# Optimization experiments

Measured on AMD Instinct MI355X. Metric: run time of the kernel, lower is better.

## Reference

```python
import jax, jax.numpy as jnp
import numpy as np

B, S, D, N, K = 2, 2048, 512, 32768, 64
CHUNK = 2048  # min(2048, num_slots) as in the torch source
EPS = 1e-8


def _phase_linear(x, Wr, Wi, br, bi):
    # complex linear on [..., d, 2] phase tensors
    xr, xi = x[..., 0], x[..., 1]
    yr = xr @ Wr.T - xi @ Wi.T + br
    yi = xr @ Wi.T + xi @ Wr.T + bi
    return jnp.stack([yr, yi], axis=-1)


def _phase_norm(x, gamma):
    # RMS normalization of the complex magnitude over dim, scaled by gamma
    mag2 = (x * x).sum(-1)                      # [..., d]
    rms = jnp.sqrt(mag2.mean(-1, keepdims=True) + EPS)
    return x * (gamma / rms)[..., None]


def setup_inputs() -> dict:
    key = jax.random.key(0)
    ks = jax.random.split(key, 8)
    inp = {
        'query': jax.random.normal(ks[0], (B, S, D, 2), jnp.float32),
        'keys': jax.random.normal(ks[1], (N, D, 2), jnp.float32) * 0.02,
        'values': jax.random.normal(ks[2], (N, D, 2), jnp.float32) * 0.02,
        'Wq_r': jax.random.normal(ks[3], (D, D), jnp.float32) * 0.02,
        'Wq_i': jax.random.normal(ks[4], (D, D), jnp.float32) * 0.02,
        'bq_r': jnp.zeros((D,), jnp.float32),
        'bq_i': jnp.zeros((D,), jnp.float32),
        'Wo_r': jax.random.normal(ks[5], (D, D), jnp.float32) * 0.02,
        'Wo_i': jax.random.normal(ks[6], (D, D), jnp.float32) * 0.02,
        'bo_r': jnp.zeros((D,), jnp.float32),
        'bo_i': jnp.zeros((D,), jnp.float32),
        'ln_gamma': jnp.ones((D,), jnp.float32),
        'top_k': K,
    }
    return inp


def _read(query, keys, values, Wq_r, Wq_i, bq_r, bq_i, Wo_r, Wo_i, bo_r, bo_i, ln_gamma, top_k):
    b, s, d, _ = query.shape
    n = keys.shape[0]
    q = _phase_linear(query, Wq_r, Wq_i, bq_r, bq_i)
    qf = q.reshape(b * s, d, 2)
    q_r, q_i = qf[..., 0], qf[..., 1]
    q_mag = jnp.sqrt((q_r * q_r + q_i * q_i).sum(-1) + EPS)  # [Q]
    nq = b * s

    n_chunks = n // CHUNK
    key_chunks = keys.reshape(n_chunks, CHUNK, d, 2)
    offsets = jnp.arange(n_chunks, dtype=jnp.int32) * CHUNK
    local_idx = jnp.arange(CHUNK, dtype=jnp.int32)

    def body(carry, xs):
        tv, ti = carry                      # [Q, K], [Q, K]
        ck, off = xs                        # [C, d, 2], scalar
        k_r, k_i = ck[..., 0], ck[..., 1]
        k_mag = jnp.sqrt((k_r * k_r + k_i * k_i).sum(-1) + EPS)   # [C]
        coh = q_r @ k_r.T + q_i @ k_i.T                            # [Q, C]
        coh = coh / (q_mag[:, None] * k_mag[None, :] + EPS)
        idx = jnp.broadcast_to(off + local_idx, (nq, CHUNK))
        cv = jnp.concatenate([tv, coh], axis=-1)
        ci = jnp.concatenate([ti, idx], axis=-1)
        nv, loc = jax.lax.top_k(cv, top_k)
        ni = jnp.take_along_axis(ci, loc, axis=-1)
        return (nv, ni), None

    init = (jnp.full((nq, top_k), -jnp.inf, jnp.float32),
            jnp.zeros((nq, top_k), jnp.int32))
    (topk_vals, topk_idx), _ = jax.lax.scan(body, init, (key_chunks, offsets))

    attn = jax.nn.softmax(topk_vals, axis=-1)                      # [Q, K]
    gathered = values[topk_idx]                                    # [Q, K, d, 2]
    retrieved = jnp.einsum('qk,qkdp->qdp', attn, gathered).reshape(b, s, d, 2)

    out = _phase_norm(retrieved, ln_gamma)
    out = _phase_linear(out, Wo_r, Wo_i, bo_r, bo_i)
    return out


def reference(query, keys, values, Wq_r, Wq_i, bq_r, bq_i, Wo_r, Wo_i, bo_r, bo_i, ln_gamma, top_k):
    return _read(query, keys, values, Wq_r, Wq_i, bq_r, bq_i, Wo_r, Wo_i, bo_r, bo_i, ln_gamma, top_k)
```

## Files before the change

### kernel.cpp

```cpp
#include <hip/hip_runtime.h>
#include <math.h>
#include <float.h>

#define EPSF 1e-8f
#define EPSD 1e-8
#define D_DIM 512
#define T_DIM 1024
#define K_TOP 64
#define K_KEEP 128
#define NBIN 2048
#define CAND_SORT 1024

typedef __bf16 bf16_t;
typedef __bf16 bf16x8 __attribute__((ext_vector_type(8)));
typedef __bf16 bf16x4 __attribute__((ext_vector_type(4)));
typedef float f32x4 __attribute__((ext_vector_type(4)));

__global__ __launch_bounds__(256)
void rownorm_convert_q_kernel(const double* __restrict__ X, double* __restrict__ magd,
                              bf16_t* __restrict__ Qn, int rows) {
  int r = blockIdx.x;
  if (r >= rows) return;
  int tid = threadIdx.x;
  const double* xr = X + (size_t)r * T_DIM;
  double v[4];
  double s = 0.0;
  #pragma unroll
  for (int i = 0; i < 4; i++) { v[i] = xr[tid * 4 + i]; s += v[i] * v[i]; }
  for (int o = 32; o > 0; o >>= 1) s += __shfl_down(s, o, 64);
  __shared__ double red[4];
  __shared__ double mag_s;
  if ((tid & 63) == 0) red[tid >> 6] = s;
  __syncthreads();
  if (tid == 0) {
    double m = sqrt(red[0] + red[1] + red[2] + red[3] + EPSD);
    magd[r] = m; mag_s = m;
  }
  __syncthreads();
  double inv = 1.0 / mag_s;
  bf16x4 o;
  #pragma unroll
  for (int i = 0; i < 4; i++) o[i] = (bf16_t)((float)(v[i] * inv));
  *(bf16x4*)(Qn + (size_t)r * T_DIM + tid * 4) = o;
}

__global__ __launch_bounds__(256)
void rownorm_convert_k_kernel(const float* __restrict__ X, double* __restrict__ magd,
                              bf16_t* __restrict__ Kn, int rows) {
  int r = blockIdx.x;
  if (r >= rows) return;
  int tid = threadIdx.x;
  float4 v = ((const float4*)(X + (size_t)r * T_DIM))[tid];
  double s = (double)v.x * v.x + (double)v.y * v.y + (double)v.z * v.z + (double)v.w * v.w;
  for (int o = 32; o > 0; o >>= 1) s += __shfl_down(s, o, 64);
  __shared__ double red[4];
  __shared__ float inv_s;
  if ((tid & 63) == 0) red[tid >> 6] = s;
  __syncthreads();
  if (tid == 0) {
    double m = sqrt(red[0] + red[1] + red[2] + red[3] + EPSD);
    magd[r] = m; inv_s = (float)(1.0 / m);
  }
  __syncthreads();
  float inv = inv_s;
  bf16x4 o;
  o[0] = (bf16_t)(v.x * inv); o[1] = (bf16_t)(v.y * inv);
  o[2] = (bf16_t)(v.z * inv); o[3] = (bf16_t)(v.w * inv);
  *(bf16x4*)(Kn + (size_t)r * T_DIM + tid * 4) = o;
}

__global__ __launch_bounds__(256)
void cgemm_f64_kernel(const float* __restrict__ X,
                      const float* __restrict__ Wr, const float* __restrict__ Wi,
                      const float* __restrict__ br, const float* __restrict__ bi,
                      double* __restrict__ Yd, int M) {
  __shared__ float Ar[16][64], Ai[16][64], Br_[16][64], Bi_[16][64];
  int tid = threadIdx.x;
  int tx = tid & 15, ty = tid >> 4;
  int m0 = blockIdx.x * 64, n0 = blockIdx.y * 64;
  double accR[4][4] = {{0}}, accI[4][4] = {{0}};
  for (int k0 = 0; k0 < D_DIM; k0 += 16) {
    #pragma unroll
    for (int gi = 0; gi < 2; gi++) {
      int g = tid + gi * 256;
      int m = g >> 3, dg = g & 7;
      float4 v = *(const float4*)(X + (size_t)(m0 + m) * T_DIM + 2 * k0 + dg * 4);
      Ar[dg*2][m] = v.x; Ai[dg*2][m] = v.y; Ar[dg*2+1][m] = v.z; Ai[dg*2+1][m] = v.w;
    }
    {
      int j = tid >> 2, c = tid & 3;
      float4 vr = *(const float4*)(Wr + (size_t)(n0 + j) * D_DIM + k0 + c * 4);
      float4 vi = *(const float4*)(Wi + (size_t)(n0 + j) * D_DIM + k0 + c * 4);
      Br_[c*4+0][j] = vr.x; Br_[c*4+1][j] = vr.y; Br_[c*4+2][j] = vr.z; Br_[c*4+3][j] = vr.w;
      Bi_[c*4+0][j] = vi.x; Bi_[c*4+1][j] = vi.y; Bi_[c*4+2][j] = vi.z; Bi_[c*4+3][j] = vi.w;
    }
    __syncthreads();
    #pragma unroll
    for (int k = 0; k < 16; k++) {
      float arr[4], aii[4], wrr[4], wii[4];
      *(float4*)arr = *(const float4*)&Ar[k][ty*4];
      *(float4*)aii = *(const float4*)&Ai[k][ty*4];
      *(float4*)wrr = *(const float4*)&Br_[k][tx*4];
      *(float4*)wii = *(const float4*)&Bi_[k][tx*4];
      #pragma unroll
      for (int im = 0; im < 4; im++)
        #pragma unroll
        for (int jn = 0; jn < 4; jn++) {
          double ar = (double)arr[im], ai = (double)aii[im];
          double wr = (double)wrr[jn], wi = (double)wii[jn];
          accR[im][jn] += ar * wr - ai * wi;
          accI[im][jn] += ar * wi + ai * wr;
        }
    }
    __syncthreads();
  }
  #pragma unroll
  for (int im = 0; im < 4; im++) {
    int m = m0 + ty * 4 + im;
    #pragma unroll
    for (int jn = 0; jn < 4; jn++) {
      int j = n0 + tx * 4 + jn;
      size_t base = (size_t)m * T_DIM + j * 2;
      Yd[base]     = accR[im][jn] + (double)br[j];
      Yd[base + 1] = accI[im][jn] + (double)bi[j];
    }
  }
}

__global__ __launch_bounds__(256)
void cgemm_kernel(const float* __restrict__ X,
                  const float* __restrict__ Wr, const float* __restrict__ Wi,
                  const float* __restrict__ br, const float* __restrict__ bi,
                  float* __restrict__ Y, int M) {
  __shared__ float Ar[16][64], Ai[16][64], Br_[16][64], Bi_[16][64];
  int tid = threadIdx.x;
  int tx = tid & 15, ty = tid >> 4;
  int m0 = blockIdx.x * 64, n0 = blockIdx.y * 64;
  float accR[4][4] = {{0}}, accI[4][4] = {{0}};
  for (int k0 = 0; k0 < D_DIM; k0 += 16) {
    #pragma unroll
    for (int gi = 0; gi < 2; gi++) {
      int g = tid + gi * 256;
      int m = g >> 3, dg = g & 7;
      float4 v = *(const float4*)(X + (size_t)(m0 + m) * T_DIM + 2 * k0 + dg * 4);
      Ar[dg*2][m] = v.x; Ai[dg*2][m] = v.y; Ar[dg*2+1][m] = v.z; Ai[dg*2+1][m] = v.w;
    }
    {
      int j = tid >> 2, c = tid & 3;
      float4 vr = *(const float4*)(Wr + (size_t)(n0 + j) * D_DIM + k0 + c * 4);
      float4 vi = *(const float4*)(Wi + (size_t)(n0 + j) * D_DIM + k0 + c * 4);
      Br_[c*4+0][j] = vr.x; Br_[c*4+1][j] = vr.y; Br_[c*4+2][j] = vr.z; Br_[c*4+3][j] = vr.w;
      Bi_[c*4+0][j] = vi.x; Bi_[c*4+1][j] = vi.y; Bi_[c*4+2][j] = vi.z; Bi_[c*4+3][j] = vi.w;
    }
    __syncthreads();
    #pragma unroll
    for (int k = 0; k < 16; k++) {
      float arr[4], aii[4], wrr[4], wii[4];
      *(float4*)arr = *(const float4*)&Ar[k][ty*4];
      *(float4*)aii = *(const float4*)&Ai[k][ty*4];
      *(float4*)wrr = *(const float4*)&Br_[k][tx*4];
      *(float4*)wii = *(const float4*)&Bi_[k][tx*4];
      #pragma unroll
      for (int im = 0; im < 4; im++)
        #pragma unroll
        for (int jn = 0; jn < 4; jn++) {
          accR[im][jn] += arr[im] * wrr[jn] - aii[im] * wii[jn];
          accI[im][jn] += arr[im] * wii[jn] + aii[im] * wrr[jn];
        }
    }
    __syncthreads();
  }
  #pragma unroll
  for (int im = 0; im < 4; im++) {
    int m = m0 + ty * 4 + im;
    #pragma unroll
    for (int jn = 0; jn < 4; jn++) {
      int j = n0 + tx * 4 + jn;
      float2 o; o.x = accR[im][jn] + br[j]; o.y = accI[im][jn] + bi[j];
      *(float2*)(Y + (size_t)m * T_DIM + j * 2) = o;
    }
  }
}

__global__ __launch_bounds__(256)
void mfma_score_kernel(const bf16_t* __restrict__ Qn, const bf16_t* __restrict__ Kn,
                       bf16_t* __restrict__ S, int n_off, int C) {
  __shared__ bf16_t As[128 * 32];
  __shared__ bf16_t Bs[128 * 32];
  int tid = threadIdx.x;
  int lane = tid & 63, wv = tid >> 6;
  int m0 = blockIdx.x * 128;
  int n0 = blockIdx.y * 128;
  int wm = (wv & 1) * 64, wn = (wv >> 1) * 64;
  f32x4 acc[4][4] = {};
  const bf16_t* Ag = Qn + (size_t)m0 * T_DIM;
  const bf16_t* Bg = Kn + (size_t)(n_off + n0) * T_DIM;
  int frow = lane & 15;
  int fk = (lane >> 4) * 8;
  for (int k0 = 0; k0 < T_DIM; k0 += 32) {
    #pragma unroll
    for (int it = 0; it < 2; it++) {
      int rbase = (it * 4 + wv) * 16;
      int row = rbase + (lane >> 2);
      int gcol = lane & 3;
      const bf16_t* gpa = Ag + (size_t)row * T_DIM + k0 + gcol * 8;
      const bf16_t* gpb = Bg + (size_t)row * T_DIM + k0 + gcol * 8;
      bf16_t* lpa = As + rbase * 32 + lane * 8;
      bf16_t* lpb = Bs + rbase * 32 + lane * 8;
      __builtin_amdgcn_global_load_lds(
          (const __attribute__((address_space(1))) void*)gpa,
          (__attribute__((address_space(3))) void*)lpa, 16, 0, 0);
      __builtin_amdgcn_global_load_lds(
          (const __attribute__((address_space(1))) void*)gpb,
          (__attribute__((address_space(3))) void*)lpb, 16, 0, 0);
    }
    __syncthreads();
    bf16x8 a[4], b[4];
    #pragma unroll
    for (int i = 0; i < 4; i++)
      a[i] = *(const bf16x8*)(As + (wm + i * 16 + frow) * 32 + fk);
    #pragma unroll
    for (int j = 0; j < 4; j++)
      b[j] = *(const bf16x8*)(Bs + (wn + j * 16 + frow) * 32 + fk);
    #pragma unroll
    for (int i = 0; i < 4; i++)
      #pragma unroll
      for (int j = 0; j < 4; j++)
        acc[i][j] = __builtin_amdgcn_mfma_f32_16x16x32_bf16(a[i], b[j], acc[i][j], 0, 0, 0);
    __syncthreads();
  }
  int col = lane & 15, qr = (lane >> 4) * 4;
  #pragma unroll
  for (int i = 0; i < 4; i++)
    #pragma unroll
    for (int j = 0; j < 4; j++) {
      int n = n0 + wn + j * 16 + col;
      #pragma unroll
      for (int r = 0; r < 4; r++) {
        int m = m0 + wm + i * 16 + qr + r;
        S[(size_t)m * C + n] = (bf16_t)acc[i][j][r];
      }
    }
}

__global__ __launch_bounds__(256)
void select_kernel(const bf16_t* __restrict__ S, int C, int key_off,
                   float* __restrict__ cand_v, int* __restrict__ cand_i,
                   int slot_off, int nslot) {
  int q = blockIdx.x, tid = threadIdx.x;
  __shared__ unsigned hist[NBIN];
  __shared__ unsigned psum[256];
  __shared__ float bv[CAND_SORT];
  __shared__ int bi[CAND_SORT];
  __shared__ unsigned binB_s, cntGt_s, binB2_s, cnt_s;
  const bf16x8* row8 = (const bf16x8*)(S + (size_t)q * C);
  int nvec = C >> 3;

  for (int i = tid; i < NBIN; i += 256) hist[i] = 0;
  if (tid == 0) { cnt_s = 0; binB_s = 0; cntGt_s = 0; binB2_s = 0; }
  __syncthreads();
  for (int v = tid; v < nvec; v += 256) {
    bf16x8 x = row8[v];
    #pragma unroll
    for (int i = 0; i < 8; i++) {
      unsigned t = __float_as_uint((float)x[i]);
      t = (t & 0x80000000u) ? ~t : (t | 0x80000000u);
      atomicAdd(&hist[t >> 21], 1u);
    }
  }
  __syncthreads();
  unsigned sgrp = 0;
  #pragma unroll
  for (int b = 0; b < 8; b++) sgrp += hist[tid * 8 + b];
  psum[tid] = sgrp;
  __syncthreads();
  for (int off = 1; off < 256; off <<= 1) {
    unsigned v = psum[tid];
    unsigned add = (tid + off < 256) ? psum[tid + off] : 0u;
    __syncthreads();
    psum[tid] = v + add;
    __syncthreads();
  }
  if (psum[tid] >= (unsigned)K_KEEP && (tid == 255 || psum[tid + 1] < (unsigned)K_KEEP)) {
    unsigned acc = (tid == 255) ? 0u : psum[tid + 1];
    for (int b = tid * 8 + 7; b >= tid * 8; b--) {
      unsigned h = hist[b];
      if (acc + h >= (unsigned)K_KEEP) { binB_s = (unsigned)b; cntGt_s = acc; break; }
      acc += h;
    }
  }
  __syncthreads();
  unsigned B = binB_s;
  unsigned K2 = (unsigned)K_KEEP - cntGt_s;
  for (int i = tid; i < NBIN; i += 256) hist[i] = 0;
  __syncthreads();
  for (int v = tid; v < nvec; v += 256) {
    bf16x8 x = row8[v];
    #pragma unroll
    for (int i = 0; i < 8; i++) {
      unsigned t = __float_as_uint((float)x[i]);
      t = (t & 0x80000000u) ? ~t : (t | 0x80000000u);
      if ((t >> 21) == B) atomicAdd(&hist[(t >> 10) & 2047u], 1u);
    }
  }
  __syncthreads();
  unsigned sgrp2 = 0;
  #pragma unroll
  for (int b = 0; b < 8; b++) sgrp2 += hist[tid * 8 + b];
  psum[tid] = sgrp2;
  __syncthreads();
  for (int off = 1; off < 256; off <<= 1) {
    unsigned v = psum[tid];
    unsigned add = (tid + off < 256) ? psum[tid + off] : 0u;
    __syncthreads();
    psum[tid] = v + add;
    __syncthreads();
  }
  if (psum[tid] >= K2 && (tid == 255 || psum[tid + 1] < K2)) {
    unsigned acc = (tid == 255) ? 0u : psum[tid + 1];
    for (int b = tid * 8 + 7; b >= tid * 8; b--) {
      unsigned h = hist[b];
      if (acc + h >= K2) { binB2_s = (unsigned)b; break; }
      acc += h;
    }
  }
  __syncthreads();
  unsigned B2 = binB2_s;
  for (int v = tid; v < nvec; v += 256) {
    bf16x8 x = row8[v];
    #pragma unroll
    for (int i = 0; i < 8; i++) {
      float fx = (float)x[i];
      unsigned t = __float_as_uint(fx);
      t = (t & 0x80000000u) ? ~t : (t | 0x80000000u);
      unsigned bin = t >> 21;
      bool keep = (bin > B) || (bin == B && ((t >> 10) & 2047u) >= B2);
      if (keep) {
        unsigned p = atomicAdd(&cnt_s, 1u);
        if (p < (unsigned)CAND_SORT) { bv[p] = fx; bi[p] = key_off + v * 8 + i; }
      }
    }
  }
  __syncthreads();
  int cnt = (int)min(cnt_s, (unsigned)CAND_SORT);
  int n = K_KEEP; while (n < cnt) n <<= 1;
  for (int x = cnt + tid; x < n; x += 256) { bv[x] = -FLT_MAX; bi[x] = 0x7FFFFFFF; }
  for (int k = 2; k <= n; k <<= 1) {
    for (int j = k >> 1; j > 0; j >>= 1) {
      __syncthreads();
      for (int i = tid; i < n; i += 256) {
        int ixj = i ^ j;
        if (ixj > i) {
          float a = bv[i], b = bv[ixj];
          int ia = bi[i], ib = bi[ixj];
          bool a_worse = (a < b) || (a == b && ia > ib);
          bool up = ((i & k) == 0);
          if (up ? a_worse : !a_worse) {
            bv[i] = b; bv[ixj] = a; bi[i] = ib; bi[ixj] = ia;
          }
        }
      }
    }
  }
  __syncthreads();
  if (tid < K_KEEP) {
    cand_v[(size_t)q * nslot + slot_off + tid] = bv[tid];
    cand_i[(size_t)q * nslot + slot_off + tid] = bi[tid];
  }
}

__global__ __launch_bounds__(256)
void merge_kernel(const float* __restrict__ cand_v, const int* __restrict__ cand_i,
                  int nslot, int* __restrict__ topi) {
  int q = blockIdx.x, tid = threadIdx.x;
  __shared__ float bv[NBIN];
  __shared__ int bi[NBIN];
  int n = K_KEEP; while (n < nslot) n <<= 1;
  for (int i = tid; i < n; i += 256) {
    if (i < nslot) { bv[i] = cand_v[(size_t)q * nslot + i]; bi[i] = cand_i[(size_t)q * nslot + i]; }
    else { bv[i] = -FLT_MAX; bi[i] = 0x7FFFFFFF; }
  }
  for (int k = 2; k <= n; k <<= 1) {
    for (int j = k >> 1; j > 0; j >>= 1) {
      __syncthreads();
      for (int i = tid; i < n; i += 256) {
        int ixj = i ^ j;
        if (ixj > i) {
          float a = bv[i], b = bv[ixj];
          int ia = bi[i], ib = bi[ixj];
          bool a_worse = (a < b) || (a == b && ia > ib);
          bool up = ((i & k) == 0);
          if (up ? a_worse : !a_worse) {
            bv[i] = b; bv[ixj] = a; bi[i] = ib; bi[ixj] = ia;
          }
        }
      }
    }
  }
  __syncthreads();
  if (tid < K_KEEP) topi[q * K_KEEP + tid] = bi[tid];
}

__global__ __launch_bounds__(256)
void rescore_kernel(const int* __restrict__ topi,
                    const double* __restrict__ Qd,
                    const double* __restrict__ qmagd, const double* __restrict__ kmagd,
                    const float* __restrict__ Kk, const float* __restrict__ V,
                    const float* __restrict__ gamma,
                    float* __restrict__ XN) {
  int q = blockIdx.x, tid = threadIdx.x;
  __shared__ double qrow[T_DIM];
  __shared__ double cval[K_KEEP];
  __shared__ int cidx[K_KEEP];
  __shared__ float w[K_TOP];
  __shared__ int widx[K_TOP];
  __shared__ float red[4];
  for (int i = tid; i < T_DIM / 2; i += 256)
    ((double2*)qrow)[i] = ((const double2*)(Qd + (size_t)q * T_DIM))[i];
  if (tid < K_KEEP) cidx[tid] = topi[q * K_KEEP + tid];
  __syncthreads();
  double qm = qmagd[q];
  int wv = tid >> 6, ln = tid & 63;
  #pragma unroll 2
  for (int c = wv; c < K_KEEP; c += 4) {
    int key = cidx[c];
    const float4* kr4 = (const float4*)(Kk + (size_t)key * T_DIM);
    double s = 0.0;
    #pragma unroll
    for (int it = 0; it < 4; it++) {
      float4 v = kr4[ln + it * 64];
      int t = (ln + it * 64) * 4;
      s += (double)v.x * qrow[t]     + (double)v.y * qrow[t + 1]
         + (double)v.z * qrow[t + 2] + (double)v.w * qrow[t + 3];
    }
    for (int o = 32; o > 0; o >>= 1) s += __shfl_down(s, o, 64);
    if (ln == 0) cval[c] = s / (qm * kmagd[key] + EPSD);
  }
  __syncthreads();
  for (int k = 2; k <= K_KEEP; k <<= 1) {
    for (int j = k >> 1; j > 0; j >>= 1) {
      __syncthreads();
      if (tid < K_KEEP) {
        int i = tid, ixj = i ^ j;
        if (ixj > i) {
          double a = cval[i], b = cval[ixj];
          int ia = cidx[i], ib = cidx[ixj];
          bool a_worse = (a < b) || (a == b && ia > ib);
          bool up = ((i & k) == 0);
          if (up ? a_worse : !a_worse) {
            cval[i] = b; cval[ixj] = a; cidx[i] = ib; cidx[ixj] = ia;
          }
        }
      }
    }
  }
  __syncthreads();
  if (tid < 64) {
    double v = cval[tid];
    double m = cval[0];
    double e = exp(v - m);
    double s = e;
    for (int o = 32; o > 0; o >>= 1) s += __shfl_down(s, o, 64);
    s = __shfl(s, 0, 64);
    w[tid] = (float)(e / s);
    widx[tid] = cidx[tid];
  }
  __syncthreads();
  float4 acc = {0.f, 0.f, 0.f, 0.f};
  #pragma unroll 8
  for (int j2 = 0; j2 < 64; j2++) {
    float wj = w[j2];
    float4 v = *(const float4*)(V + (size_t)widx[j2] * T_DIM + tid * 4);
    acc.x += wj * v.x; acc.y += wj * v.y; acc.z += wj * v.z; acc.w += wj * v.w;
  }
  float ls = acc.x*acc.x + acc.y*acc.y + acc.z*acc.z + acc.w*acc.w;
  for (int o = 32; o > 0; o >>= 1) ls += __shfl_down(ls, o, 64);
  if ((tid & 63) == 0) red[tid >> 6] = ls;
  __syncthreads();
  float tot = red[0] + red[1] + red[2] + red[3];
  float rms = sqrtf(tot / (float)D_DIM + EPSF);
  float g0 = gamma[tid * 2] / rms, g1 = gamma[tid * 2 + 1] / rms;
  float4 o = { acc.x * g0, acc.y * g0, acc.z * g1, acc.w * g1 };
  *(float4*)(XN + (size_t)q * T_DIM + tid * 4) = o;
}

extern "C" void kernel_launch(void* const* d_in, const int* in_sizes, int n_in,
                              void* d_out, int out_size, void* d_ws, size_t ws_size,
                              hipStream_t stream) {
  const float* query  = (const float*)d_in[0];
  const float* keys   = (const float*)d_in[1];
  const float* values = (const float*)d_in[2];
  const float* Wq_r   = (const float*)d_in[3];
  const float* Wq_i   = (const float*)d_in[4];
  const float* bq_r   = (const float*)d_in[5];
  const float* bq_i   = (const float*)d_in[6];
  const float* Wo_r   = (const float*)d_in[7];
  const float* Wo_i   = (const float*)d_in[8];
  const float* bo_r   = (const float*)d_in[9];
  const float* bo_i   = (const float*)d_in[10];
  const float* gamma  = (const float*)d_in[11];
  float* out = (float*)d_out;

  int M = in_sizes[0] / T_DIM;
  int N = in_sizes[1] / T_DIM;

  char* ws = (char*)d_ws;
  size_t off = 0;
  double* qd    = (double*)(ws + off); off += (size_t)M * T_DIM * 8;
  float*  xn    = (float*) (ws + off); off += (size_t)M * T_DIM * 4;
  double* qmagd = (double*)(ws + off); off += (size_t)M * 8;
  double* kmagd = (double*)(ws + off); off += (size_t)N * 8;
  int*    topi  = (int*)   (ws + off); off += (size_t)M * K_KEEP * 4;
  bf16_t* qn    = (bf16_t*)(ws + off); off += (size_t)M * T_DIM * 2;
  bf16_t* kn    = (bf16_t*)(ws + off); off += (size_t)N * T_DIM * 2;

  int C = 2048;
  for (int c = N; c >= 2048; c >>= 1) {
    size_t need = off + (size_t)M * c * 2
                + 2 * (size_t)M * (size_t)(N / c) * K_KEEP * 4;
    if (need <= ws_size) { C = c; break; }
  }
  if (C > N) C = N;
  int nchunks = N / C;
  int nslot = nchunks * K_KEEP;

  bf16_t* sc    = (bf16_t*)(ws + off); off += (size_t)M * C * 2;
  float*  candv = (float*) (ws + off); off += (size_t)M * nslot * 4;
  int*    candi = (int*)   (ws + off); off += (size_t)M * nslot * 4;

  dim3 blk(256);
  cgemm_f64_kernel<<<dim3(M / 64, D_DIM / 64), blk, 0, stream>>>(query, Wq_r, Wq_i, bq_r, bq_i, qd, M);
  rownorm_convert_q_kernel<<<dim3(M), blk, 0, stream>>>(qd, qmagd, qn, M);
  rownorm_convert_k_kernel<<<dim3(N), blk, 0, stream>>>(keys, kmagd, kn, N);
  for (int c = 0; c < nchunks; c++) {
    int noff = c * C;
    mfma_score_kernel<<<dim3(M / 128, C / 128), blk, 0, stream>>>(qn, kn, sc, noff, C);
    select_kernel<<<dim3(M), blk, 0, stream>>>(sc, C, noff, candv, candi, c * K_KEEP, nslot);
  }
  merge_kernel<<<dim3(M), blk, 0, stream>>>(candv, candi, nslot, topi);
  rescore_kernel<<<dim3(M), blk, 0, stream>>>(topi, qd, qmagd, kmagd, keys, values, gamma, xn);
  cgemm_kernel<<<dim3(M / 64, D_DIM / 64), blk, 0, stream>>>(xn, Wo_r, Wo_i, bo_r, bo_i, out, M);
}
```

Before: 1.867 ms.

## Swizzle score tiles per XCD, stage output via LDS, simplify select, dual-key rescore

The score GEMM remaps workgroups across XCDs for better L2 locality. It also stages the bf16 output tile in LDS so rows go out as coalesced 16-byte stores instead of scattered 2-byte writes. The select kernel replaces the two-level histogram with a row-max reduction plus a windowed 16-bit-key histogram, which usually needs one pass near the maximum. The rescore loop processes two candidate keys per wave iteration to expose more memory parallelism, and the merge kernel is skipped when there is only one chunk. The costs are 32KB of extra LDS in the score kernel, which may lower occupancy, and a select loop that can take several passes when scores are spread widely.

```diff
diff --git a/kernel.cpp b/kernel.cpp
--- a/kernel.cpp
+++ b/kernel.cpp
@@ -187,10 +187,17 @@
                        bf16_t* __restrict__ S, int n_off, int C) {
   __shared__ bf16_t As[128 * 32];
   __shared__ bf16_t Bs[128 * 32];
+  __shared__ bf16_t Cs[128 * 128];
   int tid = threadIdx.x;
   int lane = tid & 63, wv = tid >> 6;
-  int m0 = blockIdx.x * 128;
-  int n0 = blockIdx.y * 128;
+  int nwg = gridDim.x * gridDim.y;
+  int wg = blockIdx.x + blockIdx.y * gridDim.x;
+  int q8 = nwg >> 3, r8 = nwg & 7;
+  int xcd = wg & 7, sub = wg >> 3;
+  int swz = (xcd < r8 ? xcd * (q8 + 1) : r8 * (q8 + 1) + (xcd - r8) * q8) + sub;
+  int mt = swz % gridDim.x, nt = swz / gridDim.x;
+  int m0 = mt * 128;
+  int n0 = nt * 128;
   int wm = (wv & 1) * 64, wn = (wv >> 1) * 64;
   f32x4 acc[4][4] = {};
   const bf16_t* Ag = Qn + (size_t)m0 * T_DIM;
@@ -233,14 +240,19 @@
   #pragma unroll
   for (int i = 0; i < 4; i++)
     #pragma unroll
-    for (int j = 0; j < 4; j++) {
-      int n = n0 + wn + j * 16 + col;
+    for (int j = 0; j < 4; j++)
       #pragma unroll
-      for (int r = 0; r < 4; r++) {
-        int m = m0 + wm + i * 16 + qr + r;
-        S[(size_t)m * C + n] = (bf16_t)acc[i][j][r];
-      }
-    }
+      for (int r = 0; r < 4; r++)
+        Cs[(wm + i * 16 + qr + r) * 128 + (wn + j * 16 + col)] = (bf16_t)acc[i][j][r];
+  __syncthreads();
+  const float4* cs4 = (const float4*)Cs;
+  #pragma unroll
+  for (int it = 0; it < 8; it++) {
+    int idx = it * 256 + tid;
+    int row = idx >> 4;
+    int cb  = idx & 15;
+    *(float4*)((char*)S + ((size_t)(m0 + row) * C + n0) * 2 + cb * 16) = cs4[idx];
+  }
 }
 
 __global__ __launch_bounds__(256)
@@ -250,82 +262,85 @@
   int q = blockIdx.x, tid = threadIdx.x;
   __shared__ unsigned hist[NBIN];
   __shared__ unsigned psum[256];
+  __shared__ unsigned redmax[4];
   __shared__ float bv[CAND_SORT];
   __shared__ int bi[CAND_SORT];
-  __shared__ unsigned binB_s, cntGt_s, binB2_s, cnt_s;
+  __shared__ unsigned thr_s, cnt_s;
   const bf16x8* row8 = (const bf16x8*)(S + (size_t)q * C);
   int nvec = C >> 3;
 
-  for (int i = tid; i < NBIN; i += 256) hist[i] = 0;
-  if (tid == 0) { cnt_s = 0; binB_s = 0; cntGt_s = 0; binB2_s = 0; }
-  __syncthreads();
+  unsigned kmax = 0;
   for (int v = tid; v < nvec; v += 256) {
     bf16x8 x = row8[v];
     #pragma unroll
     for (int i = 0; i < 8; i++) {
       unsigned t = __float_as_uint((float)x[i]);
       t = (t & 0x80000000u) ? ~t : (t | 0x80000000u);
-      atomicAdd(&hist[t >> 21], 1u);
-    }
-  }
-  __syncthreads();
-  unsigned sgrp = 0;
-  #pragma unroll
-  for (int b = 0; b < 8; b++) sgrp += hist[tid * 8 + b];
-  psum[tid] = sgrp;
-  __syncthreads();
-  for (int off = 1; off < 256; off <<= 1) {
-    unsigned v = psum[tid];
-    unsigned add = (tid + off < 256) ? psum[tid + off] : 0u;
-    __syncthreads();
-    psum[tid] = v + add;
-    __syncthreads();
-  }
-  if (psum[tid] >= (unsigned)K_KEEP && (tid == 255 || psum[tid + 1] < (unsigned)K_KEEP)) {
-    unsigned acc = (tid == 255) ? 0u : psum[tid + 1];
-    for (int b = tid * 8 + 7; b >= tid * 8; b--) {
-      unsigned h = hist[b];
-      if (acc + h >= (unsigned)K_KEEP) { binB_s = (unsigned)b; cntGt_s = acc; break; }
-      acc += h;
-    }
-  }
-  __syncthreads();
-  unsigned B = binB_s;
-  unsigned K2 = (unsigned)K_KEEP - cntGt_s;
-  for (int i = tid; i < NBIN; i += 256) hist[i] = 0;
-  __syncthreads();
-  for (int v = tid; v < nvec; v += 256) {
-    bf16x8 x = row8[v];
-    #pragma unroll
-    for (int i = 0; i < 8; i++) {
-      unsigned t = __float_as_uint((float)x[i]);
-      t = (t & 0x80000000u) ? ~t : (t | 0x80000000u);
-      if ((t >> 21) == B) atomicAdd(&hist[(t >> 10) & 2047u], 1u);
-    }
-  }
-  __syncthreads();
-  unsigned sgrp2 = 0;
-  #pragma unroll
-  for (int b = 0; b < 8; b++) sgrp2 += hist[tid * 8 + b];
-  psum[tid] = sgrp2;
-  __syncthreads();
-  for (int off = 1; off < 256; off <<= 1) {
-    unsigned v = psum[tid];
-    unsigned add = (tid + off < 256) ? psum[tid + off] : 0u;
-    __syncthreads();
-    psum[tid] = v + add;
-    __syncthreads();
-  }
-  if (psum[tid] >= K2 && (tid == 255 || psum[tid + 1] < K2)) {
-    unsigned acc = (tid == 255) ? 0u : psum[tid + 1];
-    for (int b = tid * 8 + 7; b >= tid * 8; b--) {
-      unsigned h = hist[b];
-      if (acc + h >= K2) { binB2_s = (unsigned)b; break; }
-      acc += h;
-    }
-  }
-  __syncthreads();
-  unsigned B2 = binB2_s;
+      unsigned k = t >> 16;
+      kmax = kmax > k ? kmax : k;
+    }
+  }
+  for (int o = 32; o > 0; o >>= 1) {
+    unsigned other = (unsigned)__shfl_down((int)kmax, o, 64);
+    kmax = kmax > other ? kmax : other;
+  }
+  if ((tid & 63) == 0) redmax[tid >> 6] = kmax;
+  __syncthreads();
+  unsigned rm01 = redmax[0] > redmax[1] ? redmax[0] : redmax[1];
+  unsigned rm23 = redmax[2] > redmax[3] ? redmax[2] : redmax[3];
+  unsigned rowmax = rm01 > rm23 ? rm01 : rm23;
+
+  unsigned base = rowmax >= (unsigned)(NBIN - 1) ? rowmax - (unsigned)(NBIN - 1) : 0u;
+  unsigned cntAbove = 0;
+  unsigned thr = 0;
+  while (true) {
+    for (int i = tid; i < NBIN; i += 256) hist[i] = 0;
+    __syncthreads();
+    for (int v = tid; v < nvec; v += 256) {
+      bf16x8 x = row8[v];
+      #pragma unroll
+      for (int i = 0; i < 8; i++) {
+        unsigned t = __float_as_uint((float)x[i]);
+        t = (t & 0x80000000u) ? ~t : (t | 0x80000000u);
+        unsigned d = (t >> 16) - base;
+        if (d < (unsigned)NBIN) atomicAdd(&hist[d], 1u);
+      }
+    }
+    __syncthreads();
+    unsigned sg = 0;
+    #pragma unroll
+    for (int b = 0; b < 8; b++) sg += hist[tid * 8 + b];
+    psum[tid] = sg;
+    __syncthreads();
+    for (int off = 1; off < 256; off <<= 1) {
+      unsigned v0 = psum[tid];
+      unsigned ad = (tid + off < 256) ? psum[tid + off] : 0u;
+      __syncthreads();
+      psum[tid] = v0 + ad;
+      __syncthreads();
+    }
+    unsigned K2 = (unsigned)K_KEEP - cntAbove;
+    unsigned total = psum[0];
+    if (total >= K2) {
+      if (psum[tid] >= K2 && (tid == 255 || psum[tid + 1] < K2)) {
+        unsigned acc = (tid == 255) ? 0u : psum[tid + 1];
+        for (int b = tid * 8 + 7; b >= tid * 8; b--) {
+          acc += hist[b];
+          if (acc >= K2) { thr_s = base + (unsigned)b; break; }
+        }
+      }
+      __syncthreads();
+      thr = thr_s;
+      break;
+    }
+    cntAbove += total;
+    if (base == 0) { thr = 0; break; }
+    base = base >= (unsigned)NBIN ? base - (unsigned)NBIN : 0u;
+    __syncthreads();
+  }
+
+  if (tid == 0) cnt_s = 0;
+  __syncthreads();
   for (int v = tid; v < nvec; v += 256) {
     bf16x8 x = row8[v];
     #pragma unroll
@@ -333,9 +348,7 @@
       float fx = (float)x[i];
       unsigned t = __float_as_uint(fx);
       t = (t & 0x80000000u) ? ~t : (t | 0x80000000u);
-      unsigned bin = t >> 21;
-      bool keep = (bin > B) || (bin == B && ((t >> 10) & 2047u) >= B2);
-      if (keep) {
+      if ((t >> 16) >= thr) {
         unsigned p = atomicAdd(&cnt_s, 1u);
         if (p < (unsigned)CAND_SORT) { bv[p] = fx; bi[p] = key_off + v * 8 + i; }
       }
@@ -421,20 +434,29 @@
   __syncthreads();
   double qm = qmagd[q];
   int wv = tid >> 6, ln = tid & 63;
-  #pragma unroll 2
-  for (int c = wv; c < K_KEEP; c += 4) {
-    int key = cidx[c];
-    const float4* kr4 = (const float4*)(Kk + (size_t)key * T_DIM);
-    double s = 0.0;
+  for (int c = wv; c < K_KEEP; c += 8) {
+    int keyA = cidx[c];
+    int keyB = cidx[c + 4];
+    const float4* A4 = (const float4*)(Kk + (size_t)keyA * T_DIM);
+    const float4* B4 = (const float4*)(Kk + (size_t)keyB * T_DIM);
+    double sA = 0.0, sB = 0.0;
     #pragma unroll
     for (int it = 0; it < 4; it++) {
-      float4 v = kr4[ln + it * 64];
+      float4 va = A4[ln + it * 64];
+      float4 vb = B4[ln + it * 64];
       int t = (ln + it * 64) * 4;
-      s += (double)v.x * qrow[t]     + (double)v.y * qrow[t + 1]
-         + (double)v.z * qrow[t + 2] + (double)v.w * qrow[t + 3];
-    }
-    for (int o = 32; o > 0; o >>= 1) s += __shfl_down(s, o, 64);
-    if (ln == 0) cval[c] = s / (qm * kmagd[key] + EPSD);
+      double q0 = qrow[t], q1 = qrow[t + 1], q2 = qrow[t + 2], q3 = qrow[t + 3];
+      sA += (double)va.x * q0 + (double)va.y * q1 + (double)va.z * q2 + (double)va.w * q3;
+      sB += (double)vb.x * q0 + (double)vb.y * q1 + (double)vb.z * q2 + (double)vb.w * q3;
+    }
+    for (int o = 32; o > 0; o >>= 1) {
+      sA += __shfl_down(sA, o, 64);
+      sB += __shfl_down(sB, o, 64);
+    }
+    if (ln == 0) {
+      cval[c]     = sA / (qm * kmagd[keyA] + EPSD);
+      cval[c + 4] = sB / (qm * kmagd[keyB] + EPSD);
+    }
   }
   __syncthreads();
   for (int k = 2; k <= K_KEEP; k <<= 1) {
@@ -537,7 +559,11 @@
     mfma_score_kernel<<<dim3(M / 128, C / 128), blk, 0, stream>>>(qn, kn, sc, noff, C);
     select_kernel<<<dim3(M), blk, 0, stream>>>(sc, C, noff, candv, candi, c * K_KEEP, nslot);
   }
-  merge_kernel<<<dim3(M), blk, 0, stream>>>(candv, candi, nslot, topi);
-  rescore_kernel<<<dim3(M), blk, 0, stream>>>(topi, qd, qmagd, kmagd, keys, values, gamma, xn);
+  const int* top_src = candi;
+  if (nchunks > 1) {
+    merge_kernel<<<dim3(M), blk, 0, stream>>>(candv, candi, nslot, topi);
+    top_src = topi;
+  }
+  rescore_kernel<<<dim3(M), blk, 0, stream>>>(top_src, qd, qmagd, kmagd, keys, values, gamma, xn);
   cgemm_kernel<<<dim3(M / 64, D_DIM / 64), blk, 0, stream>>>(xn, Wo_r, Wo_i, bo_r, bo_i, out, M);
 }
```

New measurement: 1.826 ms. 1.02x faster.
